# Optimization experiments

Hardware: AMD Instinct MI355X
Metric: run time of the kernel (lower is better)

## Reference

```python
import jax, jax.numpy as jnp
import numpy as np

NUM_C, BS, L, D, M = 4096, 32, 512, 128, 50
TA, TB, TC = 0.075, 0.088, 1.0  # triangular membership params


def setup_inputs() -> dict:
    key = jax.random.key(0)
    ks = jax.random.split(key, 16)
    g = lambda i, shape, s: jax.random.normal(ks[i], shape, jnp.float32) * s
    return {
        "q": jax.random.randint(ks[0], (BS, L), 0, NUM_C),
        "r": jax.random.randint(ks[1], (BS, L), 0, 2),
        "k_emb": g(2, (NUM_C, D), 1.0),
        "Mk": g(3, (M, D), (2.0 / D) ** 0.5),
        "Mv0": g(4, (M, D), (2.0 / D) ** 0.5),
        "f_W": g(5, (D, 2 * D), (1.0 / (2 * D)) ** 0.5),
        "f_b": jnp.zeros((D,), jnp.float32),
        "a_W": g(6, (D, NUM_C + D), (1.0 / (NUM_C + D)) ** 0.5),
        "a_b": jnp.zeros((D,), jnp.float32),
        "e_W": g(7, (D, D), (2.0 / D) ** 0.5),
        "e_b": jnp.zeros((D,), jnp.float32),
        "add_W": g(8, (D, D), (2.0 / D) ** 0.5),
        "add_b": jnp.zeros((D,), jnp.float32),
        "Wih": g(9, (4 * D, D), (1.0 / D) ** 0.5),
        "Whh": g(10, (4 * D, D), (1.0 / D) ** 0.5),
        "bih": jnp.zeros((4 * D,), jnp.float32),
        "bhh": jnp.zeros((4 * D,), jnp.float32),
        "p_W": g(11, (1, D), (1.0 / D) ** 0.5),
        "p_b": jnp.zeros((1,), jnp.float32),
    }


def _forward(q, r, k_emb, Mk, Mv0, f_W, f_b, a_W, a_b, e_W, e_b,
             add_W, add_b, Wih, Whh, bih, bhh, p_W, p_b):
    B, T = q.shape
    k = k_emb[q]                                    # (B,L,D) key embeddings
    # a_embed = Linear(num_c + dim_s, dim_s) on concat(one_hot(q)*r, f):
    # split the weight so the one-hot matmul becomes a gather.
    a_Wq, a_Wf = a_W[:, :NUM_C], a_W[:, NUM_C:]
    yq = a_Wq.T[q] * r[..., None].astype(k.dtype)   # (B,L,D)

    def mem_step(Mv, xs):
        k_t, yq_t = xs                              # (B,D), (B,D)
        w = jax.nn.softmax(k_t @ Mk.T, axis=1)      # (B,M) addressing
        read = jnp.einsum('bm,bmd->bd', w, Mv)      # weighted read
        f = jnp.tanh(jnp.concatenate([read, k_t], 1) @ f_W.T + f_b)
        y = yq_t + f @ a_Wf.T + a_b                 # write content
        e = jax.nn.sigmoid(y @ e_W.T + e_b)         # erase gate
        a = jnp.tanh(y @ add_W.T + add_b)           # add vector
        Mv = Mv * (1.0 - w[:, :, None] * e[:, None, :]) + w[:, :, None] * a[:, None, :]
        return Mv, (w, f)

    Mv0b = jnp.broadcast_to(Mv0, (B, M, D))
    _, (w_all, f_all) = jax.lax.scan(
        mem_step, Mv0b, (k.transpose(1, 0, 2), yq.transpose(1, 0, 2)))
    w_all = w_all.transpose(1, 0, 2)                # (B,L,M)
    f_all = f_all.transpose(1, 0, 2)                # (B,L,D)

    # triangular membership -> ternary identity vectors {0,1,2}
    tw = jnp.maximum(jnp.minimum((w_all - TA) / (TB - TA),
                                 (TC - w_all) / (TC - TB)), 0.0)
    iv = jnp.where(tw >= 0.6, 2.0, jnp.where(tw >= 0.1, 1.0, 0.0))
    sq = jnp.sum(iv * iv, axis=2)                   # (B,L)
    dist = sq[:, :, None] + sq[:, None, :] - 2.0 * jnp.einsum('bim,bjm->bij', iv, iv)
    NEG = jnp.float32(-1e32)
    dist = jnp.where(dist > 0.0, NEG, dist)
    ut = jnp.triu(jnp.ones((T, T), bool), k=0)      # mask j >= i
    dist = jnp.where(ut[None], NEG, dist)
    idx = jnp.arange(T * T, dtype=dist.dtype).reshape(T, T)
    final = dist + idx[None]                        # (B,L,L)
    matched = jnp.max(final, axis=2) >= 0.0         # (B,L) has identical prev step
    prev = jnp.argmax(final, axis=2)                # (B,L) most recent identical t'

    # hop-LSTM: reuse hidden/cell state of previous identical timestep
    barange = jnp.arange(B)
    h0 = jnp.zeros((B, D), k.dtype)
    H0 = jnp.zeros((T, B, D), k.dtype)

    def lstm_step(carry, xs):
        h, c, H, C = carry
        t, f_t, m_t, p_t = xs
        h_in = jnp.where(m_t[:, None], H[p_t, barange], h)
        c_in = jnp.where(m_t[:, None], C[p_t, barange], c)
        gates = f_t @ Wih.T + bih + h_in @ Whh.T + bhh
        i_g, f_g, g_g, o_g = jnp.split(gates, 4, axis=1)  # torch order i,f,g,o
        c_new = jax.nn.sigmoid(f_g) * c_in + jax.nn.sigmoid(i_g) * jnp.tanh(g_g)
        h_new = jax.nn.sigmoid(o_g) * jnp.tanh(c_new)
        return (h_new, c_new, H.at[t].set(h_new), C.at[t].set(c_new)), h_new

    _, h_all = jax.lax.scan(
        lstm_step, (h0, h0, H0, H0),
        (jnp.arange(T), f_all.transpose(1, 0, 2), matched.T, prev.T))
    h_all = h_all.transpose(1, 0, 2)                # (B,L,D)
    # dropout is identity in eval mode
    p = jax.nn.sigmoid(h_all @ p_W.T + p_b)[..., 0]  # (B,L)
    return p


def reference(q, r, k_emb, Mk, Mv0, f_W, f_b, a_W, a_b, e_W, e_b,
              add_W, add_b, Wih, Whh, bih, bhh, p_W, p_b):
    return _forward(q, r, k_emb, Mk, Mv0, f_W, f_b, a_W, a_b, e_W, e_b,
                    add_W, add_b, Wih, Whh, bih, bhh, p_W, p_b)
```

## Files before the change

kernel.cpp:

```cpp
#include <hip/hip_runtime.h>
#include <cstdint>
#include <cstddef>

#define NUM_C 4096
#define BB 32
#define TT 512
#define DD 128
#define MM 50

using ull = unsigned long long;

__device__ __forceinline__ float sigmoidf_(float x){ return 1.0f/(1.0f + expf(-x)); }

__device__ __forceinline__ float fexp2_(float x){ return __builtin_amdgcn_exp2f(x); }
__device__ __forceinline__ float frcp_(float x){ return __builtin_amdgcn_rcpf(x); }
__device__ __forceinline__ float fast_sig_(float x){
  return frcp_(1.0f + fexp2_(-1.44269504088896341f*x));
}
__device__ __forceinline__ float fast_tanh_(float x){
  float t = fexp2_(2.88539008177792681f*x);
  return 1.0f - 2.0f*frcp_(t + 1.0f);
}

__device__ __forceinline__ float quadSum_(float v){
  int t = __builtin_amdgcn_update_dpp(0, __float_as_int(v), 0xB1, 0xF, 0xF, true);
  v += __int_as_float(t);
  t = __builtin_amdgcn_update_dpp(0, __float_as_int(v), 0x4E, 0xF, 0xF, true);
  v += __int_as_float(t);
  return v;
}

__device__ __forceinline__ void barL_(){
  asm volatile("s_waitcnt lgkmcnt(0)\n\ts_barrier" ::: "memory");
}
__device__ __forceinline__ void waitVM_(){
  asm volatile("s_waitcnt vmcnt(0)" ::: "memory");
}

__global__ __launch_bounds__(256) void kPre(
    const int* __restrict__ q, const int* __restrict__ r,
    const float* __restrict__ k_emb, const float* __restrict__ Mk,
    const float* __restrict__ f_W, const float* __restrict__ f_b,
    const float* __restrict__ a_W, const float* __restrict__ a_b,
    float* __restrict__ wAll, ull* __restrict__ keyLo, ull* __restrict__ keyHi,
    float* __restrict__ fpre, float* __restrict__ ypre)
{
  const int b = blockIdx.y, t0 = blockIdx.x * 32, tid = threadIdx.x;
  __shared__ __align__(16) float sK[32*129];
  __shared__ int sQ[32];
  __shared__ int sR[32];
  __shared__ union UU {
    struct { float sMk[MM*129]; double sZ[32*MM]; } p2;
    float sW2[128*65];
  } u;

  if (tid < 32){ sQ[tid] = q[b*TT + t0 + tid]; sR[tid] = r[b*TT + t0 + tid]; }
  __syncthreads();
  for (int i = tid; i < 32*128; i += 256){
    int tl = i >> 7, j = i & 127;
    sK[tl*129 + j] = k_emb[(size_t)sQ[tl]*DD + j];
  }
  for (int i = tid; i < MM*128; i += 256){
    int m = i >> 7, j = i & 127;
    u.p2.sMk[m*129 + j] = Mk[i];
  }
  __syncthreads();

  for (int idx = tid; idx < 32*MM; idx += 256){
    int tl = idx / MM, m = idx - tl*MM;
    double z = 0.0;
    for (int j = 0; j < DD; j++)
      z += (double)sK[tl*129 + j] * (double)u.p2.sMk[m*129 + j];
    u.p2.sZ[tl*MM + m] = z;
  }
  __syncthreads();

  {
    int tl = tid >> 3, l8 = tid & 7;
    double zmax = -1e300;
    for (int m = l8; m < MM; m += 8) zmax = fmax(zmax, u.p2.sZ[tl*MM + m]);
    for (int s = 1; s < 8; s <<= 1) zmax = fmax(zmax, __shfl_xor(zmax, s));
    double se = 0.0;
    for (int m = l8; m < MM; m += 8){
      double e = exp(u.p2.sZ[tl*MM + m] - zmax);
      u.p2.sZ[tl*MM + m] = e;
      se += e;
    }
    for (int s = 1; s < 8; s <<= 1) se += __shfl_xor(se, s);
    double inv = 1.0 / se;
    ull klo = 0, khi = 0;
    for (int m = l8; m < MM; m += 8){
      double w = u.p2.sZ[tl*MM + m] * inv;
      wAll[((size_t)(b*TT + t0 + tl))*MM + m] = (float)w;
      double tw = fmin((w - 0.075)/(0.088 - 0.075), (1.0 - w)/(1.0 - 0.088));
      tw = fmax(tw, 0.0);
      ull iv = (tw >= 0.6) ? 2ull : ((tw >= 0.1) ? 1ull : 0ull);
      if (m < 32) klo |= iv << (2*m); else khi |= iv << (2*(m-32));
    }
    for (int s = 1; s < 8; s <<= 1){ klo |= __shfl_xor(klo, s); khi |= __shfl_xor(khi, s); }
    if (l8 == 0){ keyLo[b*TT + t0 + tl] = klo; keyHi[b*TT + t0 + tl] = khi; }
  }

  {
    const int dq = tid & 31, tq = tid >> 5;
    float acc[4][4];
    #pragma unroll
    for (int a = 0; a < 4; a++){ acc[a][0]=0.f; acc[a][1]=0.f; acc[a][2]=0.f; acc[a][3]=0.f; }
    for (int jh = 0; jh < 2; jh++){
      __syncthreads();
      for (int i = tid; i < 128*64; i += 256){
        int dd = i >> 6, jj = i & 63;
        u.sW2[dd*65 + jj] = f_W[dd*256 + 128 + jh*64 + jj];
      }
      __syncthreads();
      for (int jj = 0; jj < 64; jj++){
        float kv[4], wv[4];
        #pragma unroll
        for (int a = 0; a < 4; a++) kv[a] = sK[(tq*4 + a)*129 + jh*64 + jj];
        #pragma unroll
        for (int c = 0; c < 4; c++) wv[c] = u.sW2[(dq*4 + c)*65 + jj];
        #pragma unroll
        for (int a = 0; a < 4; a++){
          acc[a][0] += kv[a]*wv[0]; acc[a][1] += kv[a]*wv[1];
          acc[a][2] += kv[a]*wv[2]; acc[a][3] += kv[a]*wv[3];
        }
      }
    }
    #pragma unroll
    for (int a = 0; a < 4; a++){
      int tl = tq*4 + a;
      #pragma unroll
      for (int c = 0; c < 4; c++){
        int d = dq*4 + c;
        fpre[((size_t)(b*TT + t0 + tl))*DD + d] = acc[a][c] + f_b[d];
      }
    }
  }

  for (int i = tid; i < 32*DD; i += 256){
    int tl = i >> 7, d = i & 127;
    ypre[((size_t)(b*TT + t0 + tl))*DD + d] =
        a_W[(size_t)d*(NUM_C + DD) + sQ[tl]] * (float)sR[tl] + a_b[d];
  }
}

__global__ __launch_bounds__(256) void kInit(
    const float* __restrict__ e_W, const float* __restrict__ add_W,
    const float* __restrict__ a_W,
    float* __restrict__ Ge, float* __restrict__ Ga,
    const float* __restrict__ Wih, float* __restrict__ Wih4)
{
  const int bx = blockIdx.x, tid = threadIdx.x;
  if (bx < 128){
    __shared__ float se[128];
    __shared__ float sa[128];
    const int d = bx;
    if (tid < 128){
      se[tid] = e_W[(size_t)d*DD + tid];
      sa[tid] = add_W[(size_t)d*DD + tid];
    }
    __syncthreads();
    if (tid < 128){
      const int k = tid;
      float ge = 0.f, ga = 0.f;
      for (int j = 0; j < DD; j++){
        float af = a_W[(size_t)j*(NUM_C + DD) + NUM_C + k];
        ge += se[j]*af;
        ga += sa[j]*af;
      }
      Ge[(size_t)d*DD + k] = ge;
      Ga[(size_t)d*DD + k] = ga;
    }
  } else {
    int idx = (bx - 128)*256 + tid;
    int j = idx >> 7, k = idx & 127;
    Wih4[(size_t)(k >> 2)*2048 + j*4 + (k & 3)] = Wih[idx];
  }
}

__global__ __launch_bounds__(256) void kEA(
    const float* __restrict__ ypre, const float* __restrict__ e_W,
    const float* __restrict__ add_W, const float* __restrict__ e_b,
    const float* __restrict__ add_b, float* __restrict__ eapre)
{
  const int jt = blockIdx.x;
  const int rt = blockIdx.y;
  const int tid = threadIdx.x;
  __shared__ float sW[64*129];
  __shared__ float sF[32*129];
  for (int i = tid; i < 64*128; i += 256){
    int jj = i >> 7, k = i & 127;
    int j = jt*64 + jj;
    sW[jj*129 + k] = (j < 128) ? e_W[(size_t)j*DD + k] : add_W[(size_t)(j-128)*DD + k];
  }
  for (int i = tid; i < 32*128; i += 256){
    int rr = i >> 7, k = i & 127;
    sF[rr*129 + k] = ypre[(size_t)(rt*32 + rr)*DD + k];
  }
  __syncthreads();
  const int jq = tid & 31, rq = tid >> 5;
  float acc[4][2];
  #pragma unroll
  for (int a = 0; a < 4; a++){ acc[a][0] = 0.f; acc[a][1] = 0.f; }
  for (int k = 0; k < 128; k++){
    float fv[4], wv[2];
    #pragma unroll
    for (int a = 0; a < 4; a++) fv[a] = sF[(rq*4 + a)*129 + k];
    wv[0] = sW[(jq*2 + 0)*129 + k];
    wv[1] = sW[(jq*2 + 1)*129 + k];
    #pragma unroll
    for (int a = 0; a < 4; a++){ acc[a][0] += fv[a]*wv[0]; acc[a][1] += fv[a]*wv[1]; }
  }
  #pragma unroll
  for (int a = 0; a < 4; a++){
    int rowi = rt*32 + rq*4 + a;
    #pragma unroll
    for (int c = 0; c < 2; c++){
      int j = jt*64 + jq*2 + c;
      float bj = (j < 128) ? e_b[j] : add_b[j - 128];
      eapre[(size_t)rowi*256 + j] = acc[a][c] + bj;
    }
  }
}

__global__ __launch_bounds__(512, 2) __attribute__((amdgpu_waves_per_eu(2, 2)))
void kFused(
    const float* __restrict__ wAll, const float* __restrict__ fpre,
    const float* __restrict__ eapre, const float* __restrict__ f_W,
    const float* __restrict__ Ge, const float* __restrict__ Ga,
    const float* __restrict__ Mv0, float* __restrict__ fAll,
    const float* __restrict__ Wih4, const float* __restrict__ bih,
    const float* __restrict__ bhh, const ull* __restrict__ keyLo,
    const ull* __restrict__ keyHi, int* __restrict__ prevA,
    const float* __restrict__ Whh, float* __restrict__ Hh,
    float* __restrict__ Ch, float* __restrict__ gpre,
    const float* __restrict__ p_W, const float* __restrict__ p_b,
    float* __restrict__ out, int* __restrict__ prog)
{
  const int tid = threadIdx.x;
  const int b = blockIdx.x & 31;
  const size_t base = (size_t)b*TT;

  __shared__ __align__(16) union SU {
    struct {
      float bufR[144]; float bufF[144]; float sW9[9*52];
      float sF8[8*128]; float sEA8[8*256]; float fO8[8*128];
    } m;
    struct { float sFc[8*128]; ull slo[TT]; ull shi[TT]; } g;
    struct {
      float xh[2][144]; float gbuf[8*512]; int spv[TT];
      float hRing[8*128]; float cRing[8*128]; float pw[DD];
    } l;
  } su;

  if (blockIdx.x < 32){
    const int dd = tid >> 2, kc = tid & 3, m0 = kc*13;
    const int wslot = (dd >> 5)*36 + (dd & 31);

    float mv[13];
    #pragma unroll
    for (int i = 0; i < 13; i++){
      int m = m0 + i;
      mv[i] = (m < MM) ? Mv0[(size_t)m*DD + dd] : 0.f;
    }
    float wf[32], ge[32], ga[32];
    {
      const float4* p;
      p = reinterpret_cast<const float4*>(&f_W[dd*256 + kc*32]);
      #pragma unroll
      for (int i = 0; i < 8; i++){ float4 v = p[i]; wf[4*i]=v.x; wf[4*i+1]=v.y; wf[4*i+2]=v.z; wf[4*i+3]=v.w; }
      p = reinterpret_cast<const float4*>(&Ge[(size_t)dd*DD + kc*32]);
      #pragma unroll
      for (int i = 0; i < 8; i++){ float4 v = p[i]; ge[4*i]=v.x; ge[4*i+1]=v.y; ge[4*i+2]=v.z; ge[4*i+3]=v.w; }
      p = reinterpret_cast<const float4*>(&Ga[(size_t)dd*DD + kc*32]);
      #pragma unroll
      for (int i = 0; i < 8; i++){ float4 v = p[i]; ga[4*i]=v.x; ga[4*i+1]=v.y; ga[4*i+2]=v.z; ga[4*i+3]=v.w; }
    }

    const int rr0 = tid / 50, mm0 = tid - rr0*50;
    if (tid < 18){ int rr = tid >> 1; su.m.sW9[rr*52 + 50 + (tid & 1)] = 0.f; }

    float4 pF = {0.f,0.f,0.f,0.f}, pEA = {0.f,0.f,0.f,0.f};
    float pW = 0.f;
    if (tid < 256) pF = reinterpret_cast<const float4*>(&fpre[base*DD])[tid];
    pEA = reinterpret_cast<const float4*>(&eapre[base*256])[tid];
    if (tid < 450) pW = wAll[(base + rr0)*MM + mm0];

    float wreg[13];

    for (int ch = 0; ch < TT/8; ch++){
      const int t0 = ch*8;
      if (ch){
        if (tid < 256){
          float4 v = reinterpret_cast<const float4*>(su.m.fO8)[tid];
          float* dst = &fAll[(base + t0 - 8)*DD + tid*4];
          __hip_atomic_store(dst+0, v.x, __ATOMIC_RELAXED, __HIP_MEMORY_SCOPE_AGENT);
          __hip_atomic_store(dst+1, v.y, __ATOMIC_RELAXED, __HIP_MEMORY_SCOPE_AGENT);
          __hip_atomic_store(dst+2, v.z, __ATOMIC_RELAXED, __HIP_MEMORY_SCOPE_AGENT);
          __hip_atomic_store(dst+3, v.w, __ATOMIC_RELAXED, __HIP_MEMORY_SCOPE_AGENT);
        }
      }
      if (tid < 256) reinterpret_cast<float4*>(su.m.sF8)[tid] = pF;
      reinterpret_cast<float4*>(su.m.sEA8)[tid] = pEA;
      if (tid < 450) su.m.sW9[rr0*52 + mm0] = pW;
      if (ch && tid < 256) waitVM_();
      if (t0 + 8 < TT){
        if (tid < 256) pF = reinterpret_cast<const float4*>(&fpre[(base + t0 + 8)*DD])[tid];
        pEA = reinterpret_cast<const float4*>(&eapre[(base + t0 + 8)*256])[tid];
        if (tid < 450) pW = (t0 + 8 + rr0 < TT) ? wAll[(base + t0 + 8 + rr0)*MM + mm0] : 0.f;
      }
      barL_();
      if (ch && tid == 0)
        __hip_atomic_store(&prog[b], ch, __ATOMIC_RELAXED, __HIP_MEMORY_SCOPE_AGENT);

      if (ch == 0){
        #pragma unroll
        for (int i = 0; i < 13; i++) wreg[i] = su.m.sW9[m0 + i];
        float r = 0.f;
        #pragma unroll
        for (int i = 0; i < 13; i++) r += wreg[i]*mv[i];
        r = quadSum_(r);
        if (kc == 0) su.m.bufR[wslot] = r;
        barL_();
      }

      #pragma unroll
      for (int tc = 0; tc < 8; tc++){
        float wn[13];
        #pragma unroll
        for (int i = 0; i < 13; i++) wn[i] = su.m.sW9[(tc+1)*52 + m0 + i];

        {
          const float4* x4 = reinterpret_cast<const float4*>(&su.m.bufR[kc*36]);
          float a0=0.f,a1=0.f,a2=0.f,a3=0.f;
          #pragma unroll
          for (int i = 0; i < 8; i++){
            float4 xv = x4[i];
            a0 += xv.x*wf[4*i]; a1 += xv.y*wf[4*i+1]; a2 += xv.z*wf[4*i+2]; a3 += xv.w*wf[4*i+3];
          }
          float s = quadSum_((a0+a1)+(a2+a3));
          float fval = fast_tanh_(s + su.m.sF8[tc*128 + dd]);
          if (kc == 0){
            su.m.bufF[wslot] = fval;
            su.m.fO8[tc*128 + dd] = fval;
          }
        }
        barL_();

        {
          const float4* x4 = reinterpret_cast<const float4*>(&su.m.bufF[kc*36]);
          float e0=0.f,e1=0.f,g0=0.f,g1=0.f;
          #pragma unroll
          for (int i = 0; i < 8; i++){
            float4 xv = x4[i];
            e0 += xv.x*ge[4*i];   e1 += xv.y*ge[4*i+1];
            e0 += xv.z*ge[4*i+2]; e1 += xv.w*ge[4*i+3];
            g0 += xv.x*ga[4*i];   g1 += xv.y*ga[4*i+1];
            g0 += xv.z*ga[4*i+2]; g1 += xv.w*ga[4*i+3];
          }
          float ep = quadSum_(e0 + e1);
          float ap = quadSum_(g0 + g1);
          float e_d = fast_sig_(ep + su.m.sEA8[tc*256 + dd]);
          float a_d = fast_tanh_(ap + su.m.sEA8[tc*256 + 128 + dd]);
          float rp0 = 0.f, rp1 = 0.f;
          #pragma unroll
          for (int i = 0; i < 13; i++){
            float t = __builtin_fmaf(-e_d, mv[i], a_d);
            mv[i] = __builtin_fmaf(wreg[i], t, mv[i]);
            if (i & 1) rp1 = __builtin_fmaf(wn[i], mv[i], rp1);
            else       rp0 = __builtin_fmaf(wn[i], mv[i], rp0);
          }
          float rd = quadSum_(rp0 + rp1);
          if (kc == 0) su.m.bufR[wslot] = rd;
        }
        #pragma unroll
        for (int i = 0; i < 13; i++) wreg[i] = wn[i];
        barL_();
      }
    }

    if (tid < 256){
      float4 v = reinterpret_cast<const float4*>(su.m.fO8)[tid];
      float* dst = &fAll[(base + TT - 8)*DD + tid*4];
      __hip_atomic_store(dst+0, v.x, __ATOMIC_RELAXED, __HIP_MEMORY_SCOPE_AGENT);
      __hip_atomic_store(dst+1, v.y, __ATOMIC_RELAXED, __HIP_MEMORY_SCOPE_AGENT);
      __hip_atomic_store(dst+2, v.z, __ATOMIC_RELAXED, __HIP_MEMORY_SCOPE_AGENT);
      __hip_atomic_store(dst+3, v.w, __ATOMIC_RELAXED, __HIP_MEMORY_SCOPE_AGENT);
      waitVM_();
    }
    __syncthreads();
    if (tid == 0)
      __hip_atomic_store(&prog[b], TT/8, __ATOMIC_RELAXED, __HIP_MEMORY_SCOPE_AGENT);

  } else if (blockIdx.x < 64){
    const float biasj = bih[tid] + bhh[tid];

    {
      su.g.slo[tid] = keyLo[base + tid];
      su.g.shi[tid] = keyHi[base + tid];
      barL_();
      const ull mylo = su.g.slo[tid], myhi = su.g.shi[tid];
      int found = -1;
      for (int j = tid - 1; j >= 0; j--){
        if (su.g.slo[j] == mylo && su.g.shi[j] == myhi){ found = j; break; }
      }
      __hip_atomic_store(&prevA[base + tid], found, __ATOMIC_RELAXED, __HIP_MEMORY_SCOPE_AGENT);
      waitVM_();
    }

    for (int ch = 0; ch < TT/8; ch++){
      const int t0 = ch*8;
      if (tid == 0){
        while (__hip_atomic_load(&prog[b], __ATOMIC_ACQUIRE, __HIP_MEMORY_SCOPE_AGENT) < ch + 1)
          __builtin_amdgcn_s_sleep(2);
      }
      __syncthreads();
      if (tid < 256){
        const float* src = &fAll[(base + t0)*DD + tid*4];
        float x0 = __hip_atomic_load(src+0, __ATOMIC_RELAXED, __HIP_MEMORY_SCOPE_AGENT);
        float x1 = __hip_atomic_load(src+1, __ATOMIC_RELAXED, __HIP_MEMORY_SCOPE_AGENT);
        float x2 = __hip_atomic_load(src+2, __ATOMIC_RELAXED, __HIP_MEMORY_SCOPE_AGENT);
        float x3 = __hip_atomic_load(src+3, __ATOMIC_RELAXED, __HIP_MEMORY_SCOPE_AGENT);
        su.g.sFc[tid*4+0] = x0; su.g.sFc[tid*4+1] = x1;
        su.g.sFc[tid*4+2] = x2; su.g.sFc[tid*4+3] = x3;
      }
      barL_();

      float acc[8];
      #pragma unroll
      for (int u = 0; u < 8; u++) acc[u] = 0.f;
      for (int k4 = 0; k4 < 32; k4++){
        float4 wv = reinterpret_cast<const float4*>(Wih4)[k4*512 + tid];
        #pragma unroll
        for (int u = 0; u < 8; u++){
          float4 fv = *reinterpret_cast<const float4*>(&su.g.sFc[u*128 + k4*4]);
          acc[u] += fv.x*wv.x; acc[u] += fv.y*wv.y;
          acc[u] += fv.z*wv.z; acc[u] += fv.w*wv.w;
        }
      }
      #pragma unroll
      for (int u = 0; u < 8; u++){
        float* dst = &gpre[(base + t0 + u)*512 + tid];
        __hip_atomic_store(dst, acc[u] + biasj, __ATOMIC_RELAXED, __HIP_MEMORY_SCOPE_AGENT);
      }
      waitVM_();
      __syncthreads();
      if (tid == 0)
        __hip_atomic_store(&prog[32 + b], ch + 1, __ATOMIC_RELAXED, __HIP_MEMORY_SCOPE_AGENT);
    }

  } else {
    const int jo = tid >> 2, kc = tid & 3;
    const int wslot = (jo >> 5)*36 + (jo & 31);

    float whh[4][32];
    #pragma unroll
    for (int g = 0; g < 4; g++){
      const float4* W4 = reinterpret_cast<const float4*>(&Whh[(size_t)(g*128 + jo)*128 + kc*32]);
      #pragma unroll
      for (int i = 0; i < 8; i++){
        float4 v = W4[i];
        whh[g][4*i] = v.x; whh[g][4*i+1] = v.y; whh[g][4*i+2] = v.z; whh[g][4*i+3] = v.w;
      }
    }

    float cin_cur = 0.f;

    for (int ch = 0; ch < TT/8; ch++){
      const int t0 = ch*8;
      if (tid == 0){
        while (__hip_atomic_load(&prog[32 + b], __ATOMIC_ACQUIRE, __HIP_MEMORY_SCOPE_AGENT) < ch + 1)
          __builtin_amdgcn_s_sleep(2);
      }
      __syncthreads();
      if (ch == 0){
        su.l.spv[tid] = __hip_atomic_load(&prevA[base + tid], __ATOMIC_RELAXED, __HIP_MEMORY_SCOPE_AGENT);
        if (tid < DD) su.l.xh[0][(tid >> 5)*36 + (tid & 31)] = 0.f;
      }
      {
        const float* src = &gpre[(base + t0)*512 + tid*8];
        float x0 = __hip_atomic_load(src+0, __ATOMIC_RELAXED, __HIP_MEMORY_SCOPE_AGENT);
        float x1 = __hip_atomic_load(src+1, __ATOMIC_RELAXED, __HIP_MEMORY_SCOPE_AGENT);
        float x2 = __hip_atomic_load(src+2, __ATOMIC_RELAXED, __HIP_MEMORY_SCOPE_AGENT);
        float x3 = __hip_atomic_load(src+3, __ATOMIC_RELAXED, __HIP_MEMORY_SCOPE_AGENT);
        float x4 = __hip_atomic_load(src+4, __ATOMIC_RELAXED, __HIP_MEMORY_SCOPE_AGENT);
        float x5 = __hip_atomic_load(src+5, __ATOMIC_RELAXED, __HIP_MEMORY_SCOPE_AGENT);
        float x6 = __hip_atomic_load(src+6, __ATOMIC_RELAXED, __HIP_MEMORY_SCOPE_AGENT);
        float x7 = __hip_atomic_load(src+7, __ATOMIC_RELAXED, __HIP_MEMORY_SCOPE_AGENT);
        float* d = &su.l.gbuf[tid*8];
        d[0]=x0; d[1]=x1; d[2]=x2; d[3]=x3; d[4]=x4; d[5]=x5; d[6]=x6; d[7]=x7;
      }
      barL_();

      #pragma unroll
      for (int tc = 0; tc < 8; tc++){
        const int t = t0 + tc, p = t & 1;
        if (tc) barL_();

        int pv2 = -1; float preH = 0.f, preC = 0.f;
        if (t + 1 < TT){
          pv2 = su.l.spv[t + 1];
          if (pv2 >= 0 && pv2 < t){
            if (pv2 >= t0){
              preH = su.l.hRing[(pv2 & 7)*128 + jo];
              preC = su.l.cRing[(pv2 & 7)*128 + jo];
            } else {
              preH = Hh[(base + pv2)*DD + jo];
              preC = Ch[(base + pv2)*DD + jo];
            }
          }
        }

        float gp0 = su.l.gbuf[tc*512 + jo];
        float gp1 = su.l.gbuf[tc*512 + 128 + jo];
        float gp2 = su.l.gbuf[tc*512 + 256 + jo];
        float gp3 = su.l.gbuf[tc*512 + 384 + jo];

        float a0=0.f,a1=0.f,a2=0.f,a3=0.f;
        {
          const float4* x4 = reinterpret_cast<const float4*>(&su.l.xh[p][kc*36]);
          #pragma unroll
          for (int i = 0; i < 8; i++){
            float4 xv = x4[i];
            a0 += xv.x*whh[0][4*i]; a0 += xv.y*whh[0][4*i+1]; a0 += xv.z*whh[0][4*i+2]; a0 += xv.w*whh[0][4*i+3];
            a1 += xv.x*whh[1][4*i]; a1 += xv.y*whh[1][4*i+1]; a1 += xv.z*whh[1][4*i+2]; a1 += xv.w*whh[1][4*i+3];
            a2 += xv.x*whh[2][4*i]; a2 += xv.y*whh[2][4*i+1]; a2 += xv.z*whh[2][4*i+2]; a2 += xv.w*whh[2][4*i+3];
            a3 += xv.x*whh[3][4*i]; a3 += xv.y*whh[3][4*i+1]; a3 += xv.z*whh[3][4*i+2]; a3 += xv.w*whh[3][4*i+3];
          }
        }
        a0 = quadSum_(a0); a1 = quadSum_(a1); a2 = quadSum_(a2); a3 = quadSum_(a3);

        const float ig = gp0 + a0, fg = gp1 + a1, gg = gp2 + a2, og = gp3 + a3;
        const float cn = fast_sig_(fg)*cin_cur + fast_sig_(ig)*fast_tanh_(gg);
        const float hn = fast_sig_(og)*fast_tanh_(cn);

        if (kc == 0){
          Hh[(base + t)*DD + jo] = hn;
          Ch[(base + t)*DD + jo] = cn;
          su.l.hRing[(t & 7)*128 + jo] = hn;
          su.l.cRing[(t & 7)*128 + jo] = cn;
        }

        float hin_n, cin_n;
        if (pv2 < 0 || pv2 >= t){ hin_n = hn; cin_n = cn; }
        else                     { hin_n = preH; cin_n = preC; }
        if (kc == 0) su.l.xh[1 - p][wslot] = hin_n;
        cin_cur = cin_n;
      }
    }

    __syncthreads();
    if (tid < DD) su.l.pw[tid] = p_W[tid];
    barL_();
    {
      const int t = tid;
      const float* hrow = &Hh[(base + t)*DD];
      float s = 0.f;
      #pragma unroll
      for (int k4 = 0; k4 < 32; k4++){
        float4 hv = *reinterpret_cast<const float4*>(&hrow[k4*4]);
        const float* wp = &su.l.pw[k4*4];
        s += hv.x*wp[0] + hv.y*wp[1] + hv.z*wp[2] + hv.w*wp[3];
      }
      out[base + t] = sigmoidf_(s + p_b[0]);
    }
  }
}

extern "C" void kernel_launch(void* const* d_in, const int* in_sizes, int n_in,
                              void* d_out, int out_size, void* d_ws, size_t ws_size,
                              hipStream_t stream) {
  const int*   q     = (const int*)  d_in[0];
  const int*   r     = (const int*)  d_in[1];
  const float* k_emb = (const float*)d_in[2];
  const float* Mk    = (const float*)d_in[3];
  const float* Mv0   = (const float*)d_in[4];
  const float* f_W   = (const float*)d_in[5];
  const float* f_b   = (const float*)d_in[6];
  const float* a_W   = (const float*)d_in[7];
  const float* a_b   = (const float*)d_in[8];
  const float* e_W   = (const float*)d_in[9];
  const float* e_b   = (const float*)d_in[10];
  const float* add_W = (const float*)d_in[11];
  const float* add_b = (const float*)d_in[12];
  const float* Wih   = (const float*)d_in[13];
  const float* Whh   = (const float*)d_in[14];
  const float* bih   = (const float*)d_in[15];
  const float* bhh   = (const float*)d_in[16];
  const float* p_W   = (const float*)d_in[17];
  const float* p_b   = (const float*)d_in[18];
  float* out = (float*)d_out;

  char* ws = (char*)d_ws;
  size_t off = 0;
  auto alloc = [&](size_t bytes) -> char* {
    char* p = ws + off;
    off += (bytes + 255) & ~(size_t)255;
    return p;
  };
  float* wAll  = (float*)alloc((size_t)BB*TT*MM*4);
  float* fpre  = (float*)alloc((size_t)BB*TT*DD*4);
  float* ypre  = (float*)alloc((size_t)BB*TT*DD*4);
  float* fAll  = (float*)alloc((size_t)BB*TT*DD*4);
  float* eapre = (float*)alloc((size_t)BB*TT*256*4);
  float* gpre  = (float*)alloc((size_t)BB*TT*512*4);
  float* Hh    = (float*)alloc((size_t)BB*TT*DD*4);
  float* Ch    = (float*)alloc((size_t)BB*TT*DD*4);
  ull*   keyLo = (ull*)  alloc((size_t)BB*TT*8);
  ull*   keyHi = (ull*)  alloc((size_t)BB*TT*8);
  int*   prevA = (int*)  alloc((size_t)BB*TT*4);
  float* Ge    = (float*)alloc((size_t)DD*DD*4);
  float* Ga    = (float*)alloc((size_t)DD*DD*4);
  float* Wih4  = (float*)alloc((size_t)512*DD*4);
  int*   prog  = (int*)  alloc(512);
  (void)ws_size; (void)in_sizes; (void)n_in; (void)out_size;

  hipMemsetAsync(prog, 0, 64*sizeof(int), stream);
  kPre  <<<dim3(16, 32), 256, 0, stream>>>(q, r, k_emb, Mk, f_W, f_b, a_W, a_b,
                                           wAll, keyLo, keyHi, fpre, ypre);
  kInit <<<384, 256, 0, stream>>>(e_W, add_W, a_W, Ge, Ga, Wih, Wih4);
  kEA   <<<dim3(4, 512), 256, 0, stream>>>(ypre, e_W, add_W, e_b, add_b, eapre);
  kFused<<<96, 512, 0, stream>>>(wAll, fpre, eapre, f_W, Ge, Ga, Mv0, fAll,
                                 Wih4, bih, bhh, keyLo, keyHi, prevA, Whh,
                                 Hh, Ch, gpre, p_W, p_b, out, prog);
}
```

Baseline: 758.5 us.

## Fold init kernel and memset into kPre, move prev-match search into LSTM blocks

Removes the separate kInit launch and the hipMemsetAsync by adding an extra row of blocks to kPre. These blocks compute Ge/Ga, the transposed Wih4 and zero the progress counters. The previous-occurrence key search moves from the gate-precompute blocks into the LSTM blocks, where it writes straight to shared memory, so the prevA global buffer and its round trip disappear. The gate blocks therefore start their chunk loop sooner, while the LSTM blocks do the O(T) scan themselves before their first wait.

```diff
diff --git a/kernel.cpp b/kernel.cpp
--- a/kernel.cpp
+++ b/kernel.cpp
@@ -37,13 +37,24 @@
   asm volatile("s_waitcnt vmcnt(0)" ::: "memory");
 }
 
+__device__ __forceinline__ float agLoad_(const float* p){
+  return __hip_atomic_load(p, __ATOMIC_RELAXED, __HIP_MEMORY_SCOPE_AGENT);
+}
+__device__ __forceinline__ void agStore_(float* p, float v){
+  __hip_atomic_store(p, v, __ATOMIC_RELAXED, __HIP_MEMORY_SCOPE_AGENT);
+}
+
 __global__ __launch_bounds__(256) void kPre(
     const int* __restrict__ q, const int* __restrict__ r,
     const float* __restrict__ k_emb, const float* __restrict__ Mk,
     const float* __restrict__ f_W, const float* __restrict__ f_b,
     const float* __restrict__ a_W, const float* __restrict__ a_b,
     float* __restrict__ wAll, ull* __restrict__ keyLo, ull* __restrict__ keyHi,
-    float* __restrict__ fpre, float* __restrict__ ypre)
+    float* __restrict__ fpre, float* __restrict__ ypre,
+    const float* __restrict__ e_W, const float* __restrict__ add_W,
+    float* __restrict__ Ge, float* __restrict__ Ga,
+    const float* __restrict__ Wih, float* __restrict__ Wih4,
+    int* __restrict__ prog)
 {
   const int b = blockIdx.y, t0 = blockIdx.x * 32, tid = threadIdx.x;
   __shared__ __align__(16) float sK[32*129];
@@ -53,6 +64,42 @@
     struct { float sMk[MM*129]; double sZ[32*MM]; } p2;
     float sW2[128*65];
   } u;
+
+  if (b == 32){
+    const int bx = blockIdx.x;
+    if (bx == 0 && tid < 96) prog[tid] = 0;
+    for (int i = tid; i < 8*128; i += 256){
+      int ld = i >> 7, j = i & 127;
+      sK[i]        = e_W  [(size_t)(bx*8 + ld)*DD + j];
+      sK[1024 + i] = add_W[(size_t)(bx*8 + ld)*DD + j];
+    }
+    __syncthreads();
+    {
+      const int ld = tid >> 5, lane = tid & 31;
+      const int d = bx*8 + ld;
+      float ge[4] = {0.f,0.f,0.f,0.f}, ga[4] = {0.f,0.f,0.f,0.f};
+      for (int j = 0; j < 128; j++){
+        float sej = sK[ld*128 + j], saj = sK[1024 + ld*128 + j];
+        #pragma unroll
+        for (int uu = 0; uu < 4; uu++){
+          float af = a_W[(size_t)j*(NUM_C + DD) + NUM_C + lane + 32*uu];
+          ge[uu] += sej*af;
+          ga[uu] += saj*af;
+        }
+      }
+      #pragma unroll
+      for (int uu = 0; uu < 4; uu++){
+        Ge[(size_t)d*DD + lane + 32*uu] = ge[uu];
+        Ga[(size_t)d*DD + lane + 32*uu] = ga[uu];
+      }
+    }
+    for (int i = tid; i < 4096; i += 256){
+      int idx = bx*4096 + i;
+      int j = idx >> 7, k = idx & 127;
+      Wih4[(size_t)(k >> 2)*2048 + j*4 + (k & 3)] = Wih[idx];
+    }
+    return;
+  }
 
   if (tid < 32){ sQ[tid] = q[b*TT + t0 + tid]; sR[tid] = r[b*TT + t0 + tid]; }
   __syncthreads();
@@ -141,40 +188,6 @@
     int tl = i >> 7, d = i & 127;
     ypre[((size_t)(b*TT + t0 + tl))*DD + d] =
         a_W[(size_t)d*(NUM_C + DD) + sQ[tl]] * (float)sR[tl] + a_b[d];
-  }
-}
-
-__global__ __launch_bounds__(256) void kInit(
-    const float* __restrict__ e_W, const float* __restrict__ add_W,
-    const float* __restrict__ a_W,
-    float* __restrict__ Ge, float* __restrict__ Ga,
-    const float* __restrict__ Wih, float* __restrict__ Wih4)
-{
-  const int bx = blockIdx.x, tid = threadIdx.x;
-  if (bx < 128){
-    __shared__ float se[128];
-    __shared__ float sa[128];
-    const int d = bx;
-    if (tid < 128){
-      se[tid] = e_W[(size_t)d*DD + tid];
-      sa[tid] = add_W[(size_t)d*DD + tid];
-    }
-    __syncthreads();
-    if (tid < 128){
-      const int k = tid;
-      float ge = 0.f, ga = 0.f;
-      for (int j = 0; j < DD; j++){
-        float af = a_W[(size_t)j*(NUM_C + DD) + NUM_C + k];
-        ge += se[j]*af;
-        ga += sa[j]*af;
-      }
-      Ge[(size_t)d*DD + k] = ge;
-      Ga[(size_t)d*DD + k] = ga;
-    }
-  } else {
-    int idx = (bx - 128)*256 + tid;
-    int j = idx >> 7, k = idx & 127;
-    Wih4[(size_t)(k >> 2)*2048 + j*4 + (k & 3)] = Wih[idx];
   }
 }
 
@@ -231,7 +244,7 @@
     const float* __restrict__ Mv0, float* __restrict__ fAll,
     const float* __restrict__ Wih4, const float* __restrict__ bih,
     const float* __restrict__ bhh, const ull* __restrict__ keyLo,
-    const ull* __restrict__ keyHi, int* __restrict__ prevA,
+    const ull* __restrict__ keyHi,
     const float* __restrict__ Whh, float* __restrict__ Hh,
     float* __restrict__ Ch, float* __restrict__ gpre,
     const float* __restrict__ p_W, const float* __restrict__ p_b,
@@ -246,7 +259,7 @@
       float bufR[144]; float bufF[144]; float sW9[9*52];
       float sF8[8*128]; float sEA8[8*256]; float fO8[8*128];
     } m;
-    struct { float sFc[8*128]; ull slo[TT]; ull shi[TT]; } g;
+    struct { float sFc[8*128]; } g;
     struct {
       float xh[2][144]; float gbuf[8*512]; int spv[TT];
       float hRing[8*128]; float cRing[8*128]; float pw[DD];
@@ -294,10 +307,8 @@
         if (tid < 256){
           float4 v = reinterpret_cast<const float4*>(su.m.fO8)[tid];
           float* dst = &fAll[(base + t0 - 8)*DD + tid*4];
-          __hip_atomic_store(dst+0, v.x, __ATOMIC_RELAXED, __HIP_MEMORY_SCOPE_AGENT);
-          __hip_atomic_store(dst+1, v.y, __ATOMIC_RELAXED, __HIP_MEMORY_SCOPE_AGENT);
-          __hip_atomic_store(dst+2, v.z, __ATOMIC_RELAXED, __HIP_MEMORY_SCOPE_AGENT);
-          __hip_atomic_store(dst+3, v.w, __ATOMIC_RELAXED, __HIP_MEMORY_SCOPE_AGENT);
+          agStore_(dst+0, v.x); agStore_(dst+1, v.y);
+          agStore_(dst+2, v.z); agStore_(dst+3, v.w);
         }
       }
       if (tid < 256) reinterpret_cast<float4*>(su.m.sF8)[tid] = pF;
@@ -382,10 +393,8 @@
     if (tid < 256){
       float4 v = reinterpret_cast<const float4*>(su.m.fO8)[tid];
       float* dst = &fAll[(base + TT - 8)*DD + tid*4];
-      __hip_atomic_store(dst+0, v.x, __ATOMIC_RELAXED, __HIP_MEMORY_SCOPE_AGENT);
-      __hip_atomic_store(dst+1, v.y, __ATOMIC_RELAXED, __HIP_MEMORY_SCOPE_AGENT);
-      __hip_atomic_store(dst+2, v.z, __ATOMIC_RELAXED, __HIP_MEMORY_SCOPE_AGENT);
-      __hip_atomic_store(dst+3, v.w, __ATOMIC_RELAXED, __HIP_MEMORY_SCOPE_AGENT);
+      agStore_(dst+0, v.x); agStore_(dst+1, v.y);
+      agStore_(dst+2, v.z); agStore_(dst+3, v.w);
       waitVM_();
     }
     __syncthreads();
@@ -394,19 +403,6 @@
 
   } else if (blockIdx.x < 64){
     const float biasj = bih[tid] + bhh[tid];
-
-    {
-      su.g.slo[tid] = keyLo[base + tid];
-      su.g.shi[tid] = keyHi[base + tid];
-      barL_();
-      const ull mylo = su.g.slo[tid], myhi = su.g.shi[tid];
-      int found = -1;
-      for (int j = tid - 1; j >= 0; j--){
-        if (su.g.slo[j] == mylo && su.g.shi[j] == myhi){ found = j; break; }
-      }
-      __hip_atomic_store(&prevA[base + tid], found, __ATOMIC_RELAXED, __HIP_MEMORY_SCOPE_AGENT);
-      waitVM_();
-    }
 
     for (int ch = 0; ch < TT/8; ch++){
       const int t0 = ch*8;
@@ -417,10 +413,8 @@
       __syncthreads();
       if (tid < 256){
         const float* src = &fAll[(base + t0)*DD + tid*4];
-        float x0 = __hip_atomic_load(src+0, __ATOMIC_RELAXED, __HIP_MEMORY_SCOPE_AGENT);
-        float x1 = __hip_atomic_load(src+1, __ATOMIC_RELAXED, __HIP_MEMORY_SCOPE_AGENT);
-        float x2 = __hip_atomic_load(src+2, __ATOMIC_RELAXED, __HIP_MEMORY_SCOPE_AGENT);
-        float x3 = __hip_atomic_load(src+3, __ATOMIC_RELAXED, __HIP_MEMORY_SCOPE_AGENT);
+        float x0 = agLoad_(src+0), x1 = agLoad_(src+1);
+        float x2 = agLoad_(src+2), x3 = agLoad_(src+3);
         su.g.sFc[tid*4+0] = x0; su.g.sFc[tid*4+1] = x1;
         su.g.sFc[tid*4+2] = x2; su.g.sFc[tid*4+3] = x3;
       }
@@ -428,21 +422,19 @@
 
       float acc[8];
       #pragma unroll
-      for (int u = 0; u < 8; u++) acc[u] = 0.f;
+      for (int uu = 0; uu < 8; uu++) acc[uu] = 0.f;
       for (int k4 = 0; k4 < 32; k4++){
         float4 wv = reinterpret_cast<const float4*>(Wih4)[k4*512 + tid];
         #pragma unroll
-        for (int u = 0; u < 8; u++){
-          float4 fv = *reinterpret_cast<const float4*>(&su.g.sFc[u*128 + k4*4]);
-          acc[u] += fv.x*wv.x; acc[u] += fv.y*wv.y;
-          acc[u] += fv.z*wv.z; acc[u] += fv.w*wv.w;
-        }
-      }
-      #pragma unroll
-      for (int u = 0; u < 8; u++){
-        float* dst = &gpre[(base + t0 + u)*512 + tid];
-        __hip_atomic_store(dst, acc[u] + biasj, __ATOMIC_RELAXED, __HIP_MEMORY_SCOPE_AGENT);
-      }
+        for (int uu = 0; uu < 8; uu++){
+          float4 fv = *reinterpret_cast<const float4*>(&su.g.sFc[uu*128 + k4*4]);
+          acc[uu] += fv.x*wv.x; acc[uu] += fv.y*wv.y;
+          acc[uu] += fv.z*wv.z; acc[uu] += fv.w*wv.w;
+        }
+      }
+      #pragma unroll
+      for (int uu = 0; uu < 8; uu++)
+        agStore_(&gpre[(base + t0 + uu)*512 + tid], acc[uu] + biasj);
       waitVM_();
       __syncthreads();
       if (tid == 0)
@@ -462,6 +454,21 @@
         float4 v = W4[i];
         whh[g][4*i] = v.x; whh[g][4*i+1] = v.y; whh[g][4*i+2] = v.z; whh[g][4*i+3] = v.w;
       }
+    }
+
+    {
+      ull* slo = reinterpret_cast<ull*>(su.l.gbuf);
+      ull* shi = slo + TT;
+      slo[tid] = keyLo[base + tid];
+      shi[tid] = keyHi[base + tid];
+      barL_();
+      const ull mylo = slo[tid], myhi = shi[tid];
+      int found = -1;
+      for (int j = tid - 1; j >= 0; j--){
+        if (slo[j] == mylo && shi[j] == myhi){ found = j; break; }
+      }
+      su.l.spv[tid] = found;
+      if (tid < DD) su.l.xh[0][(tid >> 5)*36 + (tid & 31)] = 0.f;
     }
 
     float cin_cur = 0.f;
@@ -473,20 +480,12 @@
           __builtin_amdgcn_s_sleep(2);
       }
       __syncthreads();
-      if (ch == 0){
-        su.l.spv[tid] = __hip_atomic_load(&prevA[base + tid], __ATOMIC_RELAXED, __HIP_MEMORY_SCOPE_AGENT);
-        if (tid < DD) su.l.xh[0][(tid >> 5)*36 + (tid & 31)] = 0.f;
-      }
       {
         const float* src = &gpre[(base + t0)*512 + tid*8];
-        float x0 = __hip_atomic_load(src+0, __ATOMIC_RELAXED, __HIP_MEMORY_SCOPE_AGENT);
-        float x1 = __hip_atomic_load(src+1, __ATOMIC_RELAXED, __HIP_MEMORY_SCOPE_AGENT);
-        float x2 = __hip_atomic_load(src+2, __ATOMIC_RELAXED, __HIP_MEMORY_SCOPE_AGENT);
-        float x3 = __hip_atomic_load(src+3, __ATOMIC_RELAXED, __HIP_MEMORY_SCOPE_AGENT);
-        float x4 = __hip_atomic_load(src+4, __ATOMIC_RELAXED, __HIP_MEMORY_SCOPE_AGENT);
-        float x5 = __hip_atomic_load(src+5, __ATOMIC_RELAXED, __HIP_MEMORY_SCOPE_AGENT);
-        float x6 = __hip_atomic_load(src+6, __ATOMIC_RELAXED, __HIP_MEMORY_SCOPE_AGENT);
-        float x7 = __hip_atomic_load(src+7, __ATOMIC_RELAXED, __HIP_MEMORY_SCOPE_AGENT);
+        float x0 = agLoad_(src+0), x1 = agLoad_(src+1);
+        float x2 = agLoad_(src+2), x3 = agLoad_(src+3);
+        float x4 = agLoad_(src+4), x5 = agLoad_(src+5);
+        float x6 = agLoad_(src+6), x7 = agLoad_(src+7);
         float* d = &su.l.gbuf[tid*8];
         d[0]=x0; d[1]=x1; d[2]=x2; d[3]=x3; d[4]=x4; d[5]=x5; d[6]=x6; d[7]=x7;
       }
@@ -608,19 +607,17 @@
   float* Ch    = (float*)alloc((size_t)BB*TT*DD*4);
   ull*   keyLo = (ull*)  alloc((size_t)BB*TT*8);
   ull*   keyHi = (ull*)  alloc((size_t)BB*TT*8);
-  int*   prevA = (int*)  alloc((size_t)BB*TT*4);
   float* Ge    = (float*)alloc((size_t)DD*DD*4);
   float* Ga    = (float*)alloc((size_t)DD*DD*4);
   float* Wih4  = (float*)alloc((size_t)512*DD*4);
   int*   prog  = (int*)  alloc(512);
   (void)ws_size; (void)in_sizes; (void)n_in; (void)out_size;
 
-  hipMemsetAsync(prog, 0, 64*sizeof(int), stream);
-  kPre  <<<dim3(16, 32), 256, 0, stream>>>(q, r, k_emb, Mk, f_W, f_b, a_W, a_b,
-                                           wAll, keyLo, keyHi, fpre, ypre);
-  kInit <<<384, 256, 0, stream>>>(e_W, add_W, a_W, Ge, Ga, Wih, Wih4);
+  kPre  <<<dim3(16, 33), 256, 0, stream>>>(q, r, k_emb, Mk, f_W, f_b, a_W, a_b,
+                                           wAll, keyLo, keyHi, fpre, ypre,
+                                           e_W, add_W, Ge, Ga, Wih, Wih4, prog);
   kEA   <<<dim3(4, 512), 256, 0, stream>>>(ypre, e_W, add_W, e_b, add_b, eapre);
   kFused<<<96, 512, 0, stream>>>(wAll, fpre, eapre, f_W, Ge, Ga, Mv0, fAll,
-                                 Wih4, bih, bhh, keyLo, keyHi, prevA, Whh,
+                                 Wih4, bih, bhh, keyLo, keyHi, Whh,
                                  Hh, Ch, gpre, p_W, p_b, out, prog);
 }
```

Result: no change. 756.2 us (-0.3%).
